# Kernel tuning notes

Hardware: AMD Instinct MI355X
Metric: run time of the kernel (lower is better)

Reference implementation:

```python
import jax, jax.numpy as jnp
import numpy as np

DIM = 8192
N = 8192

def setup_inputs() -> dict:
    key = jax.random.key(0)
    kx, kw = jax.random.split(key)
    x = jax.random.normal(kx, (N, DIM), dtype=jnp.float32)
    # matches nn.Parameter(torch.randn(dim) + 10)
    diagonal_weights = jax.random.normal(kw, (DIM,), dtype=jnp.float32) + 10.0
    return {"x": x, "diagonal_weights": diagonal_weights}

def reference(x, diagonal_weights):
    # x @ diag(w) == column-wise scale of x by w (identical math, O(N*d))
    return x * diagonal_weights
```

## Files before the change

kernel.cpp:

```cpp
#include <hip/hip_runtime.h>


#define DIM 8192

__global__ __launch_bounds__(256) void scale_cols_f4(
    const float4* __restrict__ x4,
    const float4* __restrict__ w4,
    float4* __restrict__ out4,
    unsigned int n4)
{
    unsigned int i = blockIdx.x * 256u + threadIdx.x;
    if (i >= n4) return;
    const unsigned int c = i & (DIM / 4 - 1);
    float4 xv = x4[i];
    float4 wv = w4[c];
    float4 o;
    o.x = xv.x * wv.x;
    o.y = xv.y * wv.y;
    o.z = xv.z * wv.z;
    o.w = xv.w * wv.w;
    out4[i] = o;
}

extern "C" void kernel_launch(void* const* d_in, const int* in_sizes, int n_in,
                              void* d_out, int out_size, void* d_ws, size_t ws_size,
                              hipStream_t stream)
{
    const float4* x4  = (const float4*)d_in[0];
    const float4* w4  = (const float4*)d_in[1];
    float4* out4      = (float4*)d_out;

    const unsigned int n4 = (unsigned int)((long long)out_size / 4);
    const unsigned int blocks = (n4 + 255u) / 256u;
    scale_cols_f4<<<blocks, 256, 0, stream>>>(x4, w4, out4, n4);
}
```

Before: 417.4 us.

## Process eight rows per thread with nontemporal loads and stores

Each block now covers a 256-column-quad slice across eight rows. Each thread loads its weight vector once and reuses it for eight rows, batching the eight loads before the eight stores. Loads and stores use nontemporal builtins so the streaming 256MB of traffic bypasses cache retention. Grid size drops eightfold and the bounds check is removed, so the kernel assumes the fixed N and DIM and is no longer general.

Result: no change. 412.1 us (-1.3%).

```diff
diff --git a/kernel.cpp b/kernel.cpp
--- a/kernel.cpp
+++ b/kernel.cpp
@@ -1,36 +1,46 @@
 #include <hip/hip_runtime.h>
 
 
+typedef float vf4 __attribute__((ext_vector_type(4)));
+
 #define DIM 8192
+#define QPR (DIM / 4)
+#define TPB 256
+#define CB_PER_ROW (QPR / TPB)
+#define ROWS_PER_BLOCK 8
 
-__global__ __launch_bounds__(256) void scale_cols_f4(
-    const float4* __restrict__ x4,
-    const float4* __restrict__ w4,
-    float4* __restrict__ out4,
-    unsigned int n4)
+__global__ __launch_bounds__(TPB) void scale_cols_f4_v2(
+    const vf4* __restrict__ x4,
+    const vf4* __restrict__ w4,
+    vf4* __restrict__ out4)
 {
-    unsigned int i = blockIdx.x * 256u + threadIdx.x;
-    if (i >= n4) return;
-    const unsigned int c = i & (DIM / 4 - 1);
-    float4 xv = x4[i];
-    float4 wv = w4[c];
-    float4 o;
-    o.x = xv.x * wv.x;
-    o.y = xv.y * wv.y;
-    o.z = xv.z * wv.z;
-    o.w = xv.w * wv.w;
-    out4[i] = o;
+    const unsigned int cb = blockIdx.x & (CB_PER_ROW - 1);
+    const unsigned int rb = blockIdx.x >> 3;
+    const unsigned int c  = cb * TPB + threadIdx.x;
+    const unsigned int r0 = rb * ROWS_PER_BLOCK;
+
+    const vf4 wv = w4[c];
+
+    const unsigned int idx = r0 * QPR + c;
+    vf4 xv[ROWS_PER_BLOCK];
+    #pragma unroll
+    for (int k = 0; k < ROWS_PER_BLOCK; ++k) {
+        xv[k] = __builtin_nontemporal_load(&x4[idx + (unsigned)k * QPR]);
+    }
+    #pragma unroll
+    for (int k = 0; k < ROWS_PER_BLOCK; ++k) {
+        __builtin_nontemporal_store(xv[k] * wv, &out4[idx + (unsigned)k * QPR]);
+    }
 }
 
 extern "C" void kernel_launch(void* const* d_in, const int* in_sizes, int n_in,
                               void* d_out, int out_size, void* d_ws, size_t ws_size,
                               hipStream_t stream)
 {
-    const float4* x4  = (const float4*)d_in[0];
-    const float4* w4  = (const float4*)d_in[1];
-    float4* out4      = (float4*)d_out;
+    const vf4* x4  = (const vf4*)d_in[0];
+    const vf4* w4  = (const vf4*)d_in[1];
+    vf4* out4      = (vf4*)d_out;
 
-    const unsigned int n4 = (unsigned int)((long long)out_size / 4);
-    const unsigned int blocks = (n4 + 255u) / 256u;
-    scale_cols_f4<<<blocks, 256, 0, stream>>>(x4, w4, out4, n4);
+    const unsigned int blocks = (8192 / ROWS_PER_BLOCK) * CB_PER_ROW;
+    scale_cols_f4_v2<<<blocks, TPB, 0, stream>>>(x4, w4, out4);
 }
```
